# Optimization experiments

Measured on AMD Instinct MI355X. Metric: run time of the kernel, lower is better.

Reference implementation:

```python
import jax, jax.numpy as jnp
import numpy as np

N_NODES = 100000
N_EDGES = 3200000
N_GRAPHS = 64
IN_FEATS = 128
DIM = 32
N_LAYERS = 4


def setup_inputs() -> dict:
    key = jax.random.key(0)
    ks = jax.random.split(key, 16)
    x = jax.random.normal(ks[0], (N_NODES, IN_FEATS), dtype=jnp.float32)
    src = jax.random.randint(ks[1], (N_EDGES,), 0, N_NODES)
    dst = jax.random.randint(ks[2], (N_EDGES,), 0, N_NODES)
    graph_ids = jnp.sort(jax.random.randint(ks[3], (N_NODES,), 0, N_GRAPHS))
    s = 1.0 / np.sqrt(IN_FEATS)
    s2 = 1.0 / np.sqrt(DIM)
    Wn0 = jax.random.uniform(ks[4], (IN_FEATS, DIM), jnp.float32, -s, s)
    bn0 = jnp.zeros((DIM,), jnp.float32)
    Ws0 = jax.random.uniform(ks[5], (IN_FEATS, DIM), jnp.float32, -s, s)
    Wn = jax.random.uniform(ks[6], (N_LAYERS - 1, DIM, DIM), jnp.float32, -s2, s2)
    bn = jnp.zeros((N_LAYERS - 1, DIM), jnp.float32)
    Ws = jax.random.uniform(ks[7], (N_LAYERS - 1, DIM, DIM), jnp.float32, -s2, s2)
    Wfc1 = jax.random.uniform(ks[8], (DIM, 8), jnp.float32, -s2, s2)
    bfc1 = jnp.zeros((8,), jnp.float32)
    Wout = jax.random.uniform(ks[9], (8, 4), jnp.float32, -1/np.sqrt(8), 1/np.sqrt(8))
    bout = jnp.zeros((4,), jnp.float32)
    return {"x": x, "Wn0": Wn0, "bn0": bn0, "Ws0": Ws0,
            "Wn": Wn, "bn": bn, "Ws": Ws,
            "Wfc1": Wfc1, "bfc1": bfc1, "Wout": Wout, "bout": bout,
            "src": src, "dst": dst, "graph_ids": graph_ids}


def _conv_layer(h, Wn_, bn_, Ws_, src, dst):
    # GraphConv(norm='none'): transform then sum over incoming edges (src -> dst)
    rhs = h @ Wn_                                   # [N, out]
    neigh = jax.ops.segment_sum(rhs[src], dst, num_segments=N_NODES) + bn_
    self_feat = h @ Ws_                             # Linear, no bias
    return jax.nn.relu(neigh + self_feat)


def reference(x, Wn0, bn0, Ws0, Wn, bn, Ws, Wfc1, bfc1, Wout, bout, src, dst, graph_ids):
    h = _conv_layer(x, Wn0, bn0, Ws0, src, dst)
    for i in range(N_LAYERS - 1):
        h = _conv_layer(h, Wn[i], bn[i], Ws[i], src, dst)
    # per-graph sum pooling (dgl.sum_nodes over batched graph)
    hg = jax.ops.segment_sum(h, graph_ids, num_segments=N_GRAPHS)  # [G, 32]
    hg2 = jax.nn.relu(hg @ Wfc1 + bfc1)
    out = jax.nn.relu(hg2 @ Wout + bout)
    return jax.nn.softmax(out, axis=1)
```

## Files before the change

### kernel.cpp

```cpp
#include <hip/hip_runtime.h>
#include <hip/hip_bf16.h>
#include <math.h>


#define TILE_NODES 256
#define CE 12800
#define SCAN_CHUNK 2048
#define MAX_NB 1024

__device__ inline unsigned char f2fp8(float f) {
    unsigned u = __float_as_uint(f);
    unsigned s = (u >> 24) & 0x80u;
    float a = fminf(fabsf(f), 448.f);
    unsigned v = __float_as_uint(a * 0x1p-120f);
    v = v + 0xFFFFFu + ((v >> 20) & 1u);
    return (unsigned char)(s | ((v >> 20) & 0x7Fu));
}
__device__ inline float fp8_dec(unsigned x) {
    unsigned v = ((x & 0x80u) << 24) | ((x & 0x7Fu) << 20);
    return __uint_as_float(v) * 0x1p120f;
}

typedef float v2f __attribute__((ext_vector_type(2)));
typedef _Float16 h2 __attribute__((ext_vector_type(2)));
typedef __fp16 p2 __attribute__((ext_vector_type(2)));
union U32H2 { unsigned u; h2 h; p2 p; };

__device__ inline unsigned packh2(float a, float b) {
#if __has_builtin(__builtin_amdgcn_cvt_pkrtz)
    U32H2 t; t.p = __builtin_amdgcn_cvt_pkrtz(a, b); return t.u;
#else
    U32H2 t; t.h.x = (_Float16)a; t.h.y = (_Float16)b; return t.u;
#endif
}
__device__ inline float dot2(unsigned a, unsigned b, float c) {
    U32H2 ua, ub; ua.u = a; ub.u = b;
#if __has_builtin(__builtin_amdgcn_fdot2)
    return __builtin_amdgcn_fdot2(ua.h, ub.h, c, false);
#else
    return c + (float)ua.h.x * (float)ub.h.x + (float)ua.h.y * (float)ub.h.y;
#endif
}

__device__ inline void acc8_fp8(unsigned w0, unsigned w1, float4& a0, float4& a1) {
#if __has_builtin(__builtin_amdgcn_cvt_pk_f32_fp8)
    v2f p0 = __builtin_amdgcn_cvt_pk_f32_fp8(w0, 0);
    v2f p1 = __builtin_amdgcn_cvt_pk_f32_fp8(w0, 1);
    v2f p2v = __builtin_amdgcn_cvt_pk_f32_fp8(w1, 0);
    v2f p3 = __builtin_amdgcn_cvt_pk_f32_fp8(w1, 1);
    a0.x += p0.x; a0.y += p0.y; a0.z += p1.x; a0.w += p1.y;
    a1.x += p2v.x; a1.y += p2v.y; a1.z += p3.x; a1.w += p3.y;
#else
    a0.x += fp8_dec(w0 & 0xFFu);         a0.y += fp8_dec((w0 >> 8) & 0xFFu);
    a0.z += fp8_dec((w0 >> 16) & 0xFFu); a0.w += fp8_dec(w0 >> 24);
    a1.x += fp8_dec(w1 & 0xFFu);         a1.y += fp8_dec((w1 >> 8) & 0xFFu);
    a1.z += fp8_dec((w1 >> 16) & 0xFFu); a1.w += fp8_dec(w1 >> 24);
#endif
}

__global__ __launch_bounds__(1024) void k_hist2(
    const int* __restrict__ dst, int* __restrict__ histT,
    int n_edges, int NB, int C)
{
    __shared__ int hist[MAX_NB];
    const int c = blockIdx.x;
    for (int b = threadIdx.x; b < NB; b += 1024) hist[b] = 0;
    __syncthreads();
    const int beg = c * CE;
    const int end = min(beg + CE, n_edges);
    for (int e = beg + threadIdx.x; e < end; e += 1024)
        atomicAdd(&hist[dst[e] >> 8], 1);
    __syncthreads();
    for (int b = threadIdx.x; b < NB; b += 1024)
        histT[b * C + c] = hist[b];
}

__global__ __launch_bounds__(256) void k_chunk_sum(
    const int* __restrict__ v, int* __restrict__ part, int n)
{
    __shared__ int red[256];
    const int base = blockIdx.x * SCAN_CHUNK;
    int s = 0;
    for (int i = threadIdx.x; i < SCAN_CHUNK; i += 256) {
        int idx = base + i;
        if (idx < n) s += v[idx];
    }
    red[threadIdx.x] = s;
    __syncthreads();
    for (int off = 128; off > 0; off >>= 1) {
        if (threadIdx.x < off) red[threadIdx.x] += red[threadIdx.x + off];
        __syncthreads();
    }
    if (threadIdx.x == 0) part[blockIdx.x] = red[0];
}

__global__ void k_scan_part(int* __restrict__ part, int nparts)
{
    if (threadIdx.x == 0 && blockIdx.x == 0) {
        int run = 0;
        for (int i = 0; i < nparts; ++i) { int v = part[i]; part[i] = run; run += v; }
    }
}

__global__ __launch_bounds__(256) void k_write_off(
    const int* __restrict__ v, const int* __restrict__ part,
    int* __restrict__ off, int n, int total)
{
    __shared__ int lds[256];
    const int tid   = threadIdx.x;
    const int base  = blockIdx.x * SCAN_CHUNK;
    const int tbase = base + tid * 8;
    int c[8];
    int tot = 0;
#pragma unroll
    for (int m = 0; m < 8; ++m) {
        int idx = tbase + m;
        c[m] = (idx < n) ? v[idx] : 0;
        tot += c[m];
    }
    lds[tid] = tot;
    __syncthreads();
    for (int o = 1; o < 256; o <<= 1) {
        int val = (tid >= o) ? lds[tid - o] : 0;
        __syncthreads();
        lds[tid] += val;
        __syncthreads();
    }
    int run = part[blockIdx.x] + lds[tid] - tot;
#pragma unroll
    for (int m = 0; m < 8; ++m) {
        int idx = tbase + m;
        if (idx < n) off[idx] = run;
        run += c[m];
    }
    if (blockIdx.x == 0 && tid == 0) off[n] = total;
}

__global__ __launch_bounds__(1024) void k_binfill(
    const int* __restrict__ src, const int* __restrict__ dst,
    const int* __restrict__ off, unsigned int* __restrict__ ebuf,
    int n_edges, int NB, int C)
{
    __shared__ int lcur[MAX_NB];
    const int c = blockIdx.x;
    for (int b = threadIdx.x; b < NB; b += 1024)
        lcur[b] = off[b * C + c];
    __syncthreads();
    const int beg = c * CE;
    const int end = min(beg + CE, n_edges);
    for (int e = beg + threadIdx.x; e < end; e += 1024) {
        const int d = dst[e];
        const int b = d >> 8;
        const unsigned int dl = (unsigned int)(d & 255);
        const int pos = atomicAdd(&lcur[b], 1);
        ebuf[pos] = (dl << 17) | (unsigned int)src[e];
    }
}

__global__ __launch_bounds__(1024) void k_tile_sort(
    const int* __restrict__ off, const unsigned int* __restrict__ ebuf,
    int* __restrict__ eidx, int* __restrict__ ptr,
    int n_nodes, int NB, int C, int n_edges)
{
    __shared__ int hist[TILE_NODES];
    __shared__ int scan[TILE_NODES];
    __shared__ int cur[TILE_NODES];
    const int t = blockIdx.x;
    const int beg = off[t * C];
    const int end = (t + 1 < NB) ? off[(t + 1) * C] : n_edges;
    const int node_base = t * TILE_NODES;
    const int n_valid = min(TILE_NODES, n_nodes - node_base);

    if (threadIdx.x < TILE_NODES) hist[threadIdx.x] = 0;
    __syncthreads();
    for (int e = beg + threadIdx.x; e < end; e += 1024)
        atomicAdd(&hist[ebuf[e] >> 17], 1);
    __syncthreads();
    if (threadIdx.x < TILE_NODES) scan[threadIdx.x] = hist[threadIdx.x];
    __syncthreads();
    for (int o = 1; o < TILE_NODES; o <<= 1) {
        int v = 0;
        if (threadIdx.x < TILE_NODES && threadIdx.x >= o) v = scan[threadIdx.x - o];
        __syncthreads();
        if (threadIdx.x < TILE_NODES) scan[threadIdx.x] += v;
        __syncthreads();
    }
    if (threadIdx.x < TILE_NODES) {
        const int ex = scan[threadIdx.x] - hist[threadIdx.x];
        cur[threadIdx.x] = ex;
        if (threadIdx.x < n_valid) ptr[node_base + threadIdx.x] = beg + ex;
    }
    if (t == NB - 1 && threadIdx.x == 0) ptr[n_nodes] = n_edges;
    __syncthreads();
    for (int e = beg + threadIdx.x; e < end; e += 1024) {
        const unsigned int v = ebuf[e];
        const int dl = (int)(v >> 17);
        const int pos = beg + atomicAdd(&cur[dl], 1);
        eidx[pos] = (int)(v & 0x1FFFFu);
    }
}

__global__ __launch_bounds__(256, 4) void k_layer0(
    const float* __restrict__ x, const float* __restrict__ Wn0,
    const float* __restrict__ bn0, const float* __restrict__ Ws0,
    unsigned char* __restrict__ Ab, float* __restrict__ B, int n_nodes)
{
    __shared__ unsigned sWn[64 * 32];
    __shared__ unsigned sWs[64 * 32];
    __shared__ unsigned sx[32 * 64];

    for (int i = threadIdx.x; i < 64 * 32; i += 256) {
        const int k2 = i >> 5, jj = i & 31;
        sWn[i] = packh2(Wn0[(2 * k2) * 32 + jj], Wn0[(2 * k2 + 1) * 32 + jj]);
        sWs[i] = packh2(Ws0[(2 * k2) * 32 + jj], Ws0[(2 * k2 + 1) * 32 + jj]);
    }
    const int tile = blockIdx.x * 32;
    {
        const float4* s4 = (const float4*)(x + (size_t)tile * 128);
        const int lim = (n_nodes - tile) * 32;
#pragma unroll
        for (int m = 0; m < 4; ++m) {
            int i = threadIdx.x + m * 256;
            if (i < lim) {
                float4 v = s4[i];
                const int row = i >> 5, q = i & 31;
                sx[row * 64 + 2 * q]     = packh2(v.x, v.y);
                sx[row * 64 + 2 * q + 1] = packh2(v.z, v.w);
            }
        }
    }
    const int j = threadIdx.x & 31;
    const int r = threadIdx.x >> 5;
    const float bias = bn0[j];
    __syncthreads();

    float accA[4] = {0.f, 0.f, 0.f, 0.f};
    float accB[4] = {bias, bias, bias, bias};
#pragma unroll 2
    for (int k2 = 0; k2 < 64; k2 += 4) {
        const unsigned wn0 = sWn[(k2 + 0) * 32 + j], ws0 = sWs[(k2 + 0) * 32 + j];
        const unsigned wn1 = sWn[(k2 + 1) * 32 + j], ws1 = sWs[(k2 + 1) * 32 + j];
        const unsigned wn2 = sWn[(k2 + 2) * 32 + j], ws2 = sWs[(k2 + 2) * 32 + j];
        const unsigned wn3 = sWn[(k2 + 3) * 32 + j], ws3 = sWs[(k2 + 3) * 32 + j];
#pragma unroll
        for (int m = 0; m < 4; ++m) {
            const uint4 xv = *(const uint4*)(sx + (r + 8 * m) * 64 + k2);
            accA[m] = dot2(xv.x, wn0, accA[m]);
            accA[m] = dot2(xv.y, wn1, accA[m]);
            accA[m] = dot2(xv.z, wn2, accA[m]);
            accA[m] = dot2(xv.w, wn3, accA[m]);
            accB[m] = dot2(xv.x, ws0, accB[m]);
            accB[m] = dot2(xv.y, ws1, accB[m]);
            accB[m] = dot2(xv.z, ws2, accB[m]);
            accB[m] = dot2(xv.w, ws3, accB[m]);
        }
    }
#pragma unroll
    for (int m = 0; m < 4; ++m) {
        const int node = tile + r + 8 * m;
        if (node < n_nodes) {
            Ab[(size_t)node * 32 + j] = f2fp8(accA[m]);
            B[(size_t)node * 32 + j] = accB[m];
        }
    }
}

__global__ __launch_bounds__(256, 4) void k_layer(
    float* HB,
    const float* __restrict__ Wn, const float* __restrict__ bnv,
    const float* __restrict__ Ws, unsigned char* __restrict__ Ab, int n_nodes)
{
    __shared__ unsigned sWn[16 * 32];
    __shared__ unsigned sWs[16 * 32];
    __shared__ unsigned sh[64 * 16];

    for (int i = threadIdx.x; i < 16 * 32; i += 256) {
        const int k2 = i >> 5, jj = i & 31;
        sWn[i] = packh2(Wn[(2 * k2) * 32 + jj], Wn[(2 * k2 + 1) * 32 + jj]);
        sWs[i] = packh2(Ws[(2 * k2) * 32 + jj], Ws[(2 * k2 + 1) * 32 + jj]);
    }
    const int tile = blockIdx.x * 64;
    {
        const float4* s4 = (const float4*)(HB + (size_t)tile * 32);
        const int lim = (n_nodes - tile) * 8;
#pragma unroll
        for (int m = 0; m < 2; ++m) {
            int i = threadIdx.x + m * 256;
            if (i < lim) {
                float4 v = s4[i];
                v.x = fmaxf(v.x, 0.f); v.y = fmaxf(v.y, 0.f);
                v.z = fmaxf(v.z, 0.f); v.w = fmaxf(v.w, 0.f);
                const int row = i >> 3, q = i & 7;
                sh[row * 16 + 2 * q]     = packh2(v.x, v.y);
                sh[row * 16 + 2 * q + 1] = packh2(v.z, v.w);
            }
        }
    }
    const int j = threadIdx.x & 31;
    const int r = threadIdx.x >> 5;
    const float bias = bnv[j];
    __syncthreads();

    float accA[8] = {0.f};
    float accB[8];
#pragma unroll
    for (int m = 0; m < 8; ++m) accB[m] = bias;
#pragma unroll 2
    for (int k2 = 0; k2 < 16; k2 += 4) {
        const unsigned wn0 = sWn[(k2 + 0) * 32 + j], ws0 = sWs[(k2 + 0) * 32 + j];
        const unsigned wn1 = sWn[(k2 + 1) * 32 + j], ws1 = sWs[(k2 + 1) * 32 + j];
        const unsigned wn2 = sWn[(k2 + 2) * 32 + j], ws2 = sWs[(k2 + 2) * 32 + j];
        const unsigned wn3 = sWn[(k2 + 3) * 32 + j], ws3 = sWs[(k2 + 3) * 32 + j];
#pragma unroll
        for (int m = 0; m < 8; ++m) {
            const uint4 hv = *(const uint4*)(sh + (r + 8 * m) * 16 + k2);
            accA[m] = dot2(hv.x, wn0, accA[m]);
            accA[m] = dot2(hv.y, wn1, accA[m]);
            accA[m] = dot2(hv.z, wn2, accA[m]);
            accA[m] = dot2(hv.w, wn3, accA[m]);
            accB[m] = dot2(hv.x, ws0, accB[m]);
            accB[m] = dot2(hv.y, ws1, accB[m]);
            accB[m] = dot2(hv.z, ws2, accB[m]);
            accB[m] = dot2(hv.w, ws3, accB[m]);
        }
    }
#pragma unroll
    for (int m = 0; m < 8; ++m) {
        const int node = tile + r + 8 * m;
        if (node < n_nodes) {
            Ab[(size_t)node * 32 + j] = f2fp8(accA[m]);
            HB[(size_t)node * 32 + j] = accB[m];
        }
    }
}

__global__ __launch_bounds__(256) void k_agg2(
    const int* __restrict__ ptr, const int* __restrict__ eidx,
    const unsigned char* __restrict__ Ab, float* __restrict__ B, int n_nodes)
{
    const int g    = blockIdx.x * 64 + (threadIdx.x >> 2);
    const int lane = threadIdx.x & 3;
    if (g >= n_nodes) return;
    const int beg = ptr[g];
    const int end = ptr[g + 1];
    const uint2* __restrict__ A2 = (const uint2*)Ab;
    float4* B4 = (float4*)B;

    float4 a0 = B4[(size_t)g * 8 + lane * 2 + 0];
    float4 a1 = B4[(size_t)g * 8 + lane * 2 + 1];
    for (int e = beg; e < end; e += 16) {
        int idx[16];
#pragma unroll
        for (int u = 0; u < 16; ++u)
            idx[u] = (e + u < end) ? eidx[e + u] : -1;
#pragma unroll
        for (int u = 0; u < 16; ++u) {
            if (idx[u] >= 0) {
                const uint2 rw = A2[(size_t)idx[u] * 4 + lane];
                acc8_fp8(rw.x, rw.y, a0, a1);
            }
        }
    }
    B4[(size_t)g * 8 + lane * 2 + 0] = a0;
    B4[(size_t)g * 8 + lane * 2 + 1] = a1;
}

__global__ __launch_bounds__(256) void k_zero_f(float* __restrict__ p, int n)
{
    int i = blockIdx.x * 256 + threadIdx.x;
    if (i < n) p[i] = 0.f;
}

__global__ __launch_bounds__(256) void k_pool1(
    const float* __restrict__ H, const int* __restrict__ gids,
    float* __restrict__ hg, int n_nodes)
{
    const int base = blockIdx.x * 128;
    const int lim  = min(base + 128, n_nodes);
    const int j = threadIdx.x & 31;
    const int r = threadIdx.x >> 5;

    int curg = -1;
    float acc = 0.f;
    for (int n = base + r; n < lim; n += 8) {
        const int g = gids[n];
        const float v = fmaxf(H[(size_t)n * 32 + j], 0.f);
        if (g != curg) {
            if (curg >= 0) atomicAdd(&hg[curg * 32 + j], acc);
            curg = g;
            acc = v;
        } else {
            acc += v;
        }
    }
    if (curg >= 0) atomicAdd(&hg[curg * 32 + j], acc);
}

__global__ __launch_bounds__(64) void k_head(
    const float* __restrict__ hg,
    const float* __restrict__ Wfc1, const float* __restrict__ bfc1,
    const float* __restrict__ Wout, const float* __restrict__ bout,
    float* __restrict__ out, int n_graphs)
{
    const int g = blockIdx.x * blockDim.x + threadIdx.x;
    if (g >= n_graphs) return;
    float h[32];
#pragma unroll
    for (int k = 0; k < 32; ++k) h[k] = hg[g * 32 + k];
    float z[8];
#pragma unroll
    for (int m = 0; m < 8; ++m) {
        float a = bfc1[m];
#pragma unroll
        for (int k = 0; k < 32; ++k) a += h[k] * Wfc1[k * 8 + m];
        z[m] = fmaxf(a, 0.f);
    }
    float o[4];
#pragma unroll
    for (int q = 0; q < 4; ++q) {
        float a = bout[q];
#pragma unroll
        for (int m = 0; m < 8; ++m) a += z[m] * Wout[m * 4 + q];
        o[q] = fmaxf(a, 0.f);
    }
    const float mx = fmaxf(fmaxf(o[0], o[1]), fmaxf(o[2], o[3]));
    const float e0 = expf(o[0] - mx), e1 = expf(o[1] - mx);
    const float e2 = expf(o[2] - mx), e3 = expf(o[3] - mx);
    const float inv = 1.f / (e0 + e1 + e2 + e3);
    out[g * 4 + 0] = e0 * inv;
    out[g * 4 + 1] = e1 * inv;
    out[g * 4 + 2] = e2 * inv;
    out[g * 4 + 3] = e3 * inv;
}

extern "C" void kernel_launch(void* const* d_in, const int* in_sizes, int n_in,
                              void* d_out, int out_size, void* d_ws, size_t ws_size,
                              hipStream_t stream)
{
    const float* x    = (const float*)d_in[0];
    const float* Wn0  = (const float*)d_in[1];
    const float* bn0  = (const float*)d_in[2];
    const float* Ws0  = (const float*)d_in[3];
    const float* Wn   = (const float*)d_in[4];
    const float* bn   = (const float*)d_in[5];
    const float* Ws   = (const float*)d_in[6];
    const float* Wfc1 = (const float*)d_in[7];
    const float* bfc1 = (const float*)d_in[8];
    const float* Wout = (const float*)d_in[9];
    const float* bout = (const float*)d_in[10];
    const int*   src  = (const int*)d_in[11];
    const int*   dst  = (const int*)d_in[12];
    const int*   gids = (const int*)d_in[13];

    const int n_nodes  = in_sizes[0] / 128;
    const int n_edges  = in_sizes[11];
    const int n_graphs = out_size / 4;
    const size_t N32 = (size_t)n_nodes * 32;

    const int NB = (n_nodes + TILE_NODES - 1) / TILE_NODES;
    const int C  = (n_edges + CE - 1) / CE;
    const int n_off = NB * C;

    unsigned char* Ab = (unsigned char*)d_ws;
    float* B   = (float*)(Ab + N32);
    float* hg  = B + N32;
    int* histT = (int*)(hg + (size_t)n_graphs * 32);
    int* off   = histT + n_off;
    int* part  = off + n_off + 1;
    int* ptr   = part + 256;
    unsigned int* ebuf = (unsigned int*)(ptr + n_nodes + 1);
    int* eidx  = (int*)(ebuf + n_edges);

    const int nparts = (n_off + SCAN_CHUNK - 1) / SCAN_CHUNK;

    k_hist2<<<C, 1024, 0, stream>>>(dst, histT, n_edges, NB, C);
    k_chunk_sum<<<nparts, 256, 0, stream>>>(histT, part, n_off);
    k_scan_part<<<1, 64, 0, stream>>>(part, nparts);
    k_write_off<<<nparts, 256, 0, stream>>>(histT, part, off, n_off, n_edges);
    k_binfill<<<C, 1024, 0, stream>>>(src, dst, off, ebuf, n_edges, NB, C);
    k_tile_sort<<<NB, 1024, 0, stream>>>(off, ebuf, eidx, ptr, n_nodes, NB, C, n_edges);

    const int mblocks0 = (n_nodes + 31) / 32;
    const int mblocks  = (n_nodes + 63) / 64;
    const int ablocks  = (n_nodes + 63) / 64;

    k_layer0<<<mblocks0, 256, 0, stream>>>(x, Wn0, bn0, Ws0, Ab, B, n_nodes);
    k_agg2<<<ablocks, 256, 0, stream>>>(ptr, eidx, Ab, B, n_nodes);

    for (int l = 0; l < 3; ++l) {
        k_layer<<<mblocks, 256, 0, stream>>>(B, Wn + l * 1024, bn + l * 32,
                                             Ws + l * 1024, Ab, n_nodes);
        k_agg2<<<ablocks, 256, 0, stream>>>(ptr, eidx, Ab, B, n_nodes);
    }

    k_zero_f<<<(n_graphs * 32 + 255) / 256, 256, 0, stream>>>(hg, n_graphs * 32);
    k_pool1<<<(n_nodes + 127) / 128, 256, 0, stream>>>(B, gids, hg, n_nodes);
    k_head<<<(n_graphs + 63) / 64, 64, 0, stream>>>(hg, Wfc1, bfc1, Wout, bout,
                                                    (float*)d_out, n_graphs);
}
```

Measured before the change: 394.9 us.

## Pad CSR rows to multiples of four with sentinel edges for vectorized index loads

The tile sort now pads each node's edge list to a multiple of four and aligns each tile's segment, writing a sentinel source index that points to a zeroed row of the fp8 feature buffer. The aggregation kernel then loads edge indices as int4 and unrolls gathers without per-edge bounds checks or validity branches. The cost is a larger edge-index array, extra sentinel gathers that add zeros, and a reserved workspace region sized for the sentinel row.

```diff
diff --git a/kernel.cpp b/kernel.cpp
--- a/kernel.cpp
+++ b/kernel.cpp
@@ -7,6 +7,7 @@
 #define CE 12800
 #define SCAN_CHUNK 2048
 #define MAX_NB 1024
+#define SENT 131071
 
 __device__ inline unsigned char f2fp8(float f) {
     unsigned u = __float_as_uint(f);
@@ -159,15 +160,17 @@
 
 __global__ __launch_bounds__(1024) void k_tile_sort(
     const int* __restrict__ off, const unsigned int* __restrict__ ebuf,
-    int* __restrict__ eidx, int* __restrict__ ptr,
+    int* __restrict__ eidx, int* __restrict__ ptrb, int* __restrict__ ptre,
     int n_nodes, int NB, int C, int n_edges)
 {
     __shared__ int hist[TILE_NODES];
+    __shared__ int phist[TILE_NODES];
     __shared__ int scan[TILE_NODES];
     __shared__ int cur[TILE_NODES];
     const int t = blockIdx.x;
     const int beg = off[t * C];
     const int end = (t + 1 < NB) ? off[(t + 1) * C] : n_edges;
+    const int tb  = ((beg + 3) & ~3) + 1024 * t;
     const int node_base = t * TILE_NODES;
     const int n_valid = min(TILE_NODES, n_nodes - node_base);
 
@@ -176,7 +179,11 @@
     for (int e = beg + threadIdx.x; e < end; e += 1024)
         atomicAdd(&hist[ebuf[e] >> 17], 1);
     __syncthreads();
-    if (threadIdx.x < TILE_NODES) scan[threadIdx.x] = hist[threadIdx.x];
+    if (threadIdx.x < TILE_NODES) {
+        const int ph = (hist[threadIdx.x] + 3) & ~3;
+        phist[threadIdx.x] = ph;
+        scan[threadIdx.x]  = ph;
+    }
     __syncthreads();
     for (int o = 1; o < TILE_NODES; o <<= 1) {
         int v = 0;
@@ -186,17 +193,25 @@
         __syncthreads();
     }
     if (threadIdx.x < TILE_NODES) {
-        const int ex = scan[threadIdx.x] - hist[threadIdx.x];
+        const int ex = scan[threadIdx.x] - phist[threadIdx.x];
         cur[threadIdx.x] = ex;
-        if (threadIdx.x < n_valid) ptr[node_base + threadIdx.x] = beg + ex;
-    }
-    if (t == NB - 1 && threadIdx.x == 0) ptr[n_nodes] = n_edges;
+        if (threadIdx.x < n_valid) {
+            ptrb[node_base + threadIdx.x] = tb + ex;
+            ptre[node_base + threadIdx.x] = tb + ex + phist[threadIdx.x];
+        }
+    }
     __syncthreads();
     for (int e = beg + threadIdx.x; e < end; e += 1024) {
         const unsigned int v = ebuf[e];
         const int dl = (int)(v >> 17);
-        const int pos = beg + atomicAdd(&cur[dl], 1);
+        const int pos = tb + atomicAdd(&cur[dl], 1);
         eidx[pos] = (int)(v & 0x1FFFFu);
+    }
+    __syncthreads();
+    if (threadIdx.x < n_valid) {
+        int p  = tb + cur[threadIdx.x];
+        const int pe = tb + scan[threadIdx.x];
+        for (; p < pe; ++p) eidx[p] = SENT;
     }
 }
 
@@ -334,32 +349,54 @@
     }
 }
 
-__global__ __launch_bounds__(256) void k_agg2(
-    const int* __restrict__ ptr, const int* __restrict__ eidx,
+__global__ __launch_bounds__(256) void k_agg3(
+    const int* __restrict__ ptrb, const int* __restrict__ ptre,
+    const int* __restrict__ eidx,
     const unsigned char* __restrict__ Ab, float* __restrict__ B, int n_nodes)
 {
     const int g    = blockIdx.x * 64 + (threadIdx.x >> 2);
     const int lane = threadIdx.x & 3;
     if (g >= n_nodes) return;
-    const int beg = ptr[g];
-    const int end = ptr[g + 1];
+    const int beg = ptrb[g];
+    const int end = ptre[g];
     const uint2* __restrict__ A2 = (const uint2*)Ab;
+    const int4* __restrict__ E4 = (const int4*)eidx;
     float4* B4 = (float4*)B;
 
     float4 a0 = B4[(size_t)g * 8 + lane * 2 + 0];
     float4 a1 = B4[(size_t)g * 8 + lane * 2 + 1];
-    for (int e = beg; e < end; e += 16) {
-        int idx[16];
-#pragma unroll
-        for (int u = 0; u < 16; ++u)
-            idx[u] = (e + u < end) ? eidx[e + u] : -1;
-#pragma unroll
-        for (int u = 0; u < 16; ++u) {
-            if (idx[u] >= 0) {
-                const uint2 rw = A2[(size_t)idx[u] * 4 + lane];
-                acc8_fp8(rw.x, rw.y, a0, a1);
-            }
-        }
+    int e4 = beg >> 2;
+    const int n4 = end >> 2;
+    for (; e4 + 4 <= n4; e4 += 4) {
+        const int4 q0 = E4[e4 + 0];
+        const int4 q1 = E4[e4 + 1];
+        const int4 q2 = E4[e4 + 2];
+        const int4 q3 = E4[e4 + 3];
+        uint2 rw;
+        rw = A2[(size_t)q0.x * 4 + lane]; acc8_fp8(rw.x, rw.y, a0, a1);
+        rw = A2[(size_t)q0.y * 4 + lane]; acc8_fp8(rw.x, rw.y, a0, a1);
+        rw = A2[(size_t)q0.z * 4 + lane]; acc8_fp8(rw.x, rw.y, a0, a1);
+        rw = A2[(size_t)q0.w * 4 + lane]; acc8_fp8(rw.x, rw.y, a0, a1);
+        rw = A2[(size_t)q1.x * 4 + lane]; acc8_fp8(rw.x, rw.y, a0, a1);
+        rw = A2[(size_t)q1.y * 4 + lane]; acc8_fp8(rw.x, rw.y, a0, a1);
+        rw = A2[(size_t)q1.z * 4 + lane]; acc8_fp8(rw.x, rw.y, a0, a1);
+        rw = A2[(size_t)q1.w * 4 + lane]; acc8_fp8(rw.x, rw.y, a0, a1);
+        rw = A2[(size_t)q2.x * 4 + lane]; acc8_fp8(rw.x, rw.y, a0, a1);
+        rw = A2[(size_t)q2.y * 4 + lane]; acc8_fp8(rw.x, rw.y, a0, a1);
+        rw = A2[(size_t)q2.z * 4 + lane]; acc8_fp8(rw.x, rw.y, a0, a1);
+        rw = A2[(size_t)q2.w * 4 + lane]; acc8_fp8(rw.x, rw.y, a0, a1);
+        rw = A2[(size_t)q3.x * 4 + lane]; acc8_fp8(rw.x, rw.y, a0, a1);
+        rw = A2[(size_t)q3.y * 4 + lane]; acc8_fp8(rw.x, rw.y, a0, a1);
+        rw = A2[(size_t)q3.z * 4 + lane]; acc8_fp8(rw.x, rw.y, a0, a1);
+        rw = A2[(size_t)q3.w * 4 + lane]; acc8_fp8(rw.x, rw.y, a0, a1);
+    }
+    for (; e4 < n4; ++e4) {
+        const int4 q = E4[e4];
+        uint2 rw;
+        rw = A2[(size_t)q.x * 4 + lane]; acc8_fp8(rw.x, rw.y, a0, a1);
+        rw = A2[(size_t)q.y * 4 + lane]; acc8_fp8(rw.x, rw.y, a0, a1);
+        rw = A2[(size_t)q.z * 4 + lane]; acc8_fp8(rw.x, rw.y, a0, a1);
+        rw = A2[(size_t)q.w * 4 + lane]; acc8_fp8(rw.x, rw.y, a0, a1);
     }
     B4[(size_t)g * 8 + lane * 2 + 0] = a0;
     B4[(size_t)g * 8 + lane * 2 + 1] = a1;
@@ -456,19 +493,21 @@
     const int n_edges  = in_sizes[11];
     const int n_graphs = out_size / 4;
     const size_t N32 = (size_t)n_nodes * 32;
+    const size_t AB_ROWS = 131072;
 
     const int NB = (n_nodes + TILE_NODES - 1) / TILE_NODES;
     const int C  = (n_edges + CE - 1) / CE;
     const int n_off = NB * C;
 
     unsigned char* Ab = (unsigned char*)d_ws;
-    float* B   = (float*)(Ab + N32);
+    float* B   = (float*)(Ab + AB_ROWS * 32);
     float* hg  = B + N32;
     int* histT = (int*)(hg + (size_t)n_graphs * 32);
     int* off   = histT + n_off;
     int* part  = off + n_off + 1;
-    int* ptr   = part + 256;
-    unsigned int* ebuf = (unsigned int*)(ptr + n_nodes + 1);
+    int* ptrb  = part + 256;
+    int* ptre  = ptrb + n_nodes;
+    unsigned int* ebuf = (unsigned int*)(ptre + n_nodes);
     int* eidx  = (int*)(ebuf + n_edges);
 
     const int nparts = (n_off + SCAN_CHUNK - 1) / SCAN_CHUNK;
@@ -478,19 +517,21 @@
     k_scan_part<<<1, 64, 0, stream>>>(part, nparts);
     k_write_off<<<nparts, 256, 0, stream>>>(histT, part, off, n_off, n_edges);
     k_binfill<<<C, 1024, 0, stream>>>(src, dst, off, ebuf, n_edges, NB, C);
-    k_tile_sort<<<NB, 1024, 0, stream>>>(off, ebuf, eidx, ptr, n_nodes, NB, C, n_edges);
+    k_tile_sort<<<NB, 1024, 0, stream>>>(off, ebuf, eidx, ptrb, ptre,
+                                         n_nodes, NB, C, n_edges);
+    k_zero_f<<<1, 256, 0, stream>>>((float*)(Ab + (size_t)SENT * 32), 8);
 
     const int mblocks0 = (n_nodes + 31) / 32;
     const int mblocks  = (n_nodes + 63) / 64;
     const int ablocks  = (n_nodes + 63) / 64;
 
     k_layer0<<<mblocks0, 256, 0, stream>>>(x, Wn0, bn0, Ws0, Ab, B, n_nodes);
-    k_agg2<<<ablocks, 256, 0, stream>>>(ptr, eidx, Ab, B, n_nodes);
+    k_agg3<<<ablocks, 256, 0, stream>>>(ptrb, ptre, eidx, Ab, B, n_nodes);
 
     for (int l = 0; l < 3; ++l) {
         k_layer<<<mblocks, 256, 0, stream>>>(B, Wn + l * 1024, bn + l * 32,
                                              Ws + l * 1024, Ab, n_nodes);
-        k_agg2<<<ablocks, 256, 0, stream>>>(ptr, eidx, Ab, B, n_nodes);
+        k_agg3<<<ablocks, 256, 0, stream>>>(ptrb, ptre, eidx, Ab, B, n_nodes);
     }
 
     k_zero_f<<<(n_graphs * 32 + 255) / 256, 256, 0, stream>>>(hg, n_graphs * 32);
```

After: 367.6 us. 1.07x faster.
